# Kernel optimization log

Hardware: AMD Instinct MI355X
Metric: run time of the kernel (lower is better)

## Reference

```python
import jax, jax.numpy as jnp
import numpy as np

N, T = 4, 2048
FEAT, VEC = 512, 16          # feat_size, vec_size
K = 8192                     # codebook_size = prediction_encoder.output_size
CIN = 512                    # prediction_encoder.input_size
OFFSET = 0
IGNORE = -100                # torch CrossEntropyLoss default ignore_index
EPS = 1e-12                  # torch F.normalize eps


def setup_inputs() -> dict:
    key = jax.random.key(0)
    k1, k2, k3, k4, k5, k6 = jax.random.split(key, 6)
    feats = jax.random.normal(k1, (N, T, FEAT), dtype=jnp.float32)
    context = jax.random.normal(k2, (N, T, CIN), dtype=jnp.float32)
    lens = jax.random.randint(k3, (N,), T // 2, T + 1, dtype=jnp.int32)
    # xavier_normal_ for (feat_size, vec_size)
    proj_matrix = jax.random.normal(k4, (FEAT, VEC), dtype=jnp.float32) * np.sqrt(2.0 / (FEAT + VEC))
    cb = jax.random.normal(k5, (K, VEC), dtype=jnp.float32)
    codebook = cb / jnp.maximum(jnp.linalg.norm(cb, axis=1, keepdims=True), EPS)
    W_enc = jax.random.normal(k6, (CIN, K), dtype=jnp.float32) / np.sqrt(CIN)
    b_enc = jnp.zeros((K,), dtype=jnp.float32)
    return {"feats": feats, "context": context, "lens": lens,
            "proj_matrix": proj_matrix, "codebook": codebook,
            "W_enc": W_enc, "b_enc": b_enc}


def reference(feats, context, lens, proj_matrix, codebook, W_enc, b_enc):
    # prediction encoder: Linear(CIN -> K), lens unchanged
    logits = jnp.einsum("ntc,ck->ntk", context, W_enc) + b_enc      # (N,T,K)

    # --- target computation (no_grad in torch) ---
    f = feats[:, OFFSET:] @ proj_matrix                              # (N,T',V)
    f = f / jnp.maximum(jnp.linalg.norm(f, axis=-1, keepdims=True), EPS)
    # squared distance ||f - c||^2 = |f|^2 - 2 f.c + |c|^2; argmin equals
    # argmin of vector_norm since sqrt is monotone. Avoids (N,T,K,V) tensor.
    d2 = (jnp.sum(f * f, axis=-1, keepdims=True)
          - 2.0 * jnp.einsum("ntv,kv->ntk", f, codebook)
          + jnp.sum(codebook * codebook, axis=-1))                   # (N,T',K)
    targets = jnp.argmin(d2, axis=2).astype(jnp.int32)               # (N,T')
    Tp = T - OFFSET
    mask = (lens[:, None] - OFFSET) > jnp.arange(Tp)[None, :]        # (N,T')
    targets = jnp.where(mask, targets, IGNORE)

    # --- masked cross entropy (mean over non-ignored) ---
    logits_f = logits[:, OFFSET:].reshape(-1, K)                     # (N*T',K)
    targets_f = targets.reshape(-1)
    logp = jax.nn.log_softmax(logits_f, axis=-1)
    valid = targets_f != IGNORE
    safe_t = jnp.where(valid, targets_f, 0)
    nll = -jnp.take_along_axis(logp, safe_t[:, None], axis=1)[:, 0]
    loss = jnp.sum(nll * valid) / jnp.maximum(jnp.sum(valid), 1)
    return loss
```

## Files before the change

### kernel.cpp

```cpp
#include <hip/hip_runtime.h>
#include <hip/hip_bf16.h>
#include <hip/hip_fp8.h>

#define MROWS 8192
#define KDIM  512
#define NCOL  8192
#define TSEQ  2048

typedef float f32x4 __attribute__((ext_vector_type(4)));

__device__ __forceinline__ unsigned int pack4_fp8(float a, float b, float c, float d) {
#if __has_builtin(__builtin_amdgcn_cvt_pk_fp8_f32)
  int r = __builtin_amdgcn_cvt_pk_fp8_f32(a, b, 0, false);
  r = __builtin_amdgcn_cvt_pk_fp8_f32(c, d, r, true);
  return (unsigned int)r;
#else
  __hip_fp8_e4m3 ha(a), hb(b), hc(c), hd(d);
  return (unsigned int)ha.__x | ((unsigned int)hb.__x << 8) |
         ((unsigned int)hc.__x << 16) | ((unsigned int)hd.__x << 24);
#endif
}

__device__ __forceinline__ float fp8d(unsigned char b) {
  unsigned int s = b >> 7, e = (b >> 3) & 15, m = b & 7;
  if (e == 0) {
    float v = (float)m * 0.001953125f;
    return s ? -v : v;
  }
  unsigned int bits = (s << 31) | ((e + 120) << 23) | (m << 20);
  return __uint_as_float(bits);
}

__global__ void prep_kernel(const float* __restrict__ X, unsigned char* __restrict__ A8,
                            const float* __restrict__ W, unsigned char* __restrict__ B8,
                            const float* __restrict__ feats, const float* __restrict__ proj,
                            float* __restrict__ F, unsigned long long* __restrict__ amin,
                            float* __restrict__ rowsum) {
  __shared__ float tile[64][65];
  const int tid = threadIdx.x;
  int b = blockIdx.x;
  if (b < 4096) {
    int i = b * 256 + tid;
    float4 v = reinterpret_cast<const float4*>(X)[i];
    reinterpret_cast<unsigned int*>(A8)[i] = pack4_fp8(v.x, v.y, v.z, v.w);
  } else if (b < 5120) {
    b -= 4096;
    const int bx = b & 127, by = b >> 7;
    const int c4 = tid & 15, rr = tid >> 4;
    #pragma unroll
    for (int p = 0; p < 4; ++p) {
      int row = p * 16 + rr;
      float4 v = reinterpret_cast<const float4*>(W + (size_t)(by * 64 + row) * NCOL + bx * 64)[c4];
      tile[row][c4 * 4 + 0] = v.x; tile[row][c4 * 4 + 1] = v.y;
      tile[row][c4 * 4 + 2] = v.z; tile[row][c4 * 4 + 3] = v.w;
    }
    __syncthreads();
    #pragma unroll
    for (int p = 0; p < 4; ++p) {
      int oc = p * 16 + rr;
      unsigned int pk = pack4_fp8(tile[c4 * 4 + 0][oc], tile[c4 * 4 + 1][oc],
                                  tile[c4 * 4 + 2][oc], tile[c4 * 4 + 3][oc]);
      *reinterpret_cast<unsigned int*>(B8 + (size_t)(bx * 64 + oc) * KDIM + by * 64 + c4 * 4) = pk;
    }
  } else if (b < 5632) {
    b -= 5120;
    int rl = tid >> 4, d = tid & 15;
    int row = b * 16 + rl;
    const float4* fr4 = reinterpret_cast<const float4*>(feats + (size_t)row * KDIM);
    float acc = 0.f;
    #pragma unroll 4
    for (int kc = 0; kc < KDIM / 4; ++kc) {
      float4 v = fr4[kc];
      const float* p = proj + (size_t)kc * 64 + d;
      acc += v.x * p[0] + v.y * p[16] + v.z * p[32] + v.w * p[48];
    }
    F[(size_t)row * 16 + d] = acc;
  } else {
    int r = (b - 5632) * 256 + tid;
    amin[r] = ~0ull;
    rowsum[r] = 0.f;
  }
}

#define TGT_BLOCKS 512
#define CB_CODES 128

__device__ __forceinline__ void gld16(const void* g, void* l3) {
  __builtin_amdgcn_global_load_lds((const __attribute__((address_space(1))) void*)g,
                                   (__attribute__((address_space(3))) void*)l3, 16, 0, 0);
}

__global__ __launch_bounds__(256, 4)
void gemm_targets_kernel(const unsigned char* __restrict__ A,
                         const unsigned char* __restrict__ B,
                         const float* __restrict__ bias,
                         float* __restrict__ rowsum,
                         const float* __restrict__ F,
                         const float* __restrict__ cb,
                         unsigned long long* __restrict__ amin) {
  __shared__ __align__(16) unsigned char smem[32768];
  const int tid = threadIdx.x;
  const int bid = blockIdx.x;

  if (bid < TGT_BLOCKS) {
    float (*csh)[16] = (float (*)[16])smem;
    const int r0 = (bid & 7) * 1024 + tid;
    const int c0 = (bid >> 3) * CB_CODES;
    {
      int ci = tid >> 1, half = tid & 1;
      const float4* src = reinterpret_cast<const float4*>(cb + (size_t)(c0 + ci) * 16 + half * 8);
      float4 v0 = src[0], v1 = src[1];
      float4* dst = reinterpret_cast<float4*>(&csh[ci][half * 8]);
      dst[0] = v0; dst[1] = v1;
    }
    float4 fa[4][4];
    #pragma unroll
    for (int q = 0; q < 4; ++q) {
      const float4* fp = reinterpret_cast<const float4*>(F + (size_t)(r0 + q * 256) * 16);
      fa[q][0] = fp[0]; fa[q][1] = fp[1]; fa[q][2] = fp[2]; fa[q][3] = fp[3];
    }
    __syncthreads();

    float best[4] = {3.4e38f, 3.4e38f, 3.4e38f, 3.4e38f};
    int bidx[4] = {0, 0, 0, 0};
    #pragma unroll 2
    for (int ci = 0; ci < CB_CODES; ++ci) {
      const float4* cvp = reinterpret_cast<const float4*>(&csh[ci][0]);
      float4 c0v = cvp[0], c1v = cvp[1], c2v = cvp[2], c3v = cvp[3];
      #pragma unroll
      for (int q = 0; q < 4; ++q) {
        float dot = fa[q][0].x*c0v.x + fa[q][0].y*c0v.y + fa[q][0].z*c0v.z + fa[q][0].w*c0v.w
                  + fa[q][1].x*c1v.x + fa[q][1].y*c1v.y + fa[q][1].z*c1v.z + fa[q][1].w*c1v.w
                  + fa[q][2].x*c2v.x + fa[q][2].y*c2v.y + fa[q][2].z*c2v.z + fa[q][2].w*c2v.w
                  + fa[q][3].x*c3v.x + fa[q][3].y*c3v.y + fa[q][3].z*c3v.z + fa[q][3].w*c3v.w;
        float d = -dot;
        if (d < best[q]) { best[q] = d; bidx[q] = c0 + ci; }
      }
    }
    #pragma unroll
    for (int q = 0; q < 4; ++q) {
      unsigned int u = __float_as_uint(best[q]);
      unsigned int key = (u & 0x80000000u) ? ~u : (u | 0x80000000u);
      unsigned long long pk = ((unsigned long long)key << 32) | (unsigned int)bidx[q];
      atomicMin(&amin[r0 + q * 256], pk);
    }
    return;
  }

  const int gid = bid - TGT_BLOCKS;
  const int wave = tid >> 6;
  const int lane = tid & 63;
  const int xcd = gid & 7, idx = gid >> 3;
  const int bx = xcd * 8 + (idx & 7);
  const int by = idx >> 3;
  const int row0 = by * 128;
  const int col0 = bx * 128;
  const int wr = wave >> 1, wc = wave & 1;
  unsigned char* As = smem;
  unsigned char* Bs = smem + 16384;

  f32x4 acc[4][4];
  #pragma unroll
  for (int i = 0; i < 4; ++i)
    #pragma unroll
    for (int j = 0; j < 4; ++j) acc[i][j] = (f32x4){0.f, 0.f, 0.f, 0.f};

  const int lr = lane >> 2;
  const int lcs = (((lane & 3) ^ ((lane >> 3) & 3)) << 4);

  const int l15 = lane & 15, l16 = lane >> 4;
  const int sw = (l15 >> 1) & 3;
  const int subo = (l16 & 1) * 8;
  const int lg16 = l16 >> 1;

  #pragma unroll
  for (int c = 0; c < 2; ++c) {
    int rchunk = (wave * 2 + c) * 16;
    gld16(A + (size_t)(row0 + rchunk + lr) * KDIM + lcs, As + rchunk * 64);
    gld16(B + (size_t)(col0 + rchunk + lr) * KDIM + lcs, Bs + rchunk * 64);
  }
  __syncthreads();

  #pragma unroll
  for (int t = 0; t < 8; ++t) {
    const int cur = (t & 1) * 8192;
    if (t < 7) {
      const int kt = (t + 1) * 64;
      const int nxt = ((t + 1) & 1) * 8192;
      #pragma unroll
      for (int c = 0; c < 2; ++c) {
        int rchunk = (wave * 2 + c) * 16;
        gld16(A + (size_t)(row0 + rchunk + lr) * KDIM + kt + lcs, As + nxt + rchunk * 64);
        gld16(B + (size_t)(col0 + rchunk + lr) * KDIM + kt + lcs, Bs + nxt + rchunk * 64);
      }
    }
    #pragma unroll
    for (int ks = 0; ks < 2; ++ks) {
      const int poff = (((ks * 2 + lg16) ^ sw) << 4) + subo;
      long af[4], bb[4];
      #pragma unroll
      for (int mi = 0; mi < 4; ++mi)
        af[mi] = *(const long*)(As + cur + (wr * 64 + mi * 16 + l15) * 64 + poff);
      #pragma unroll
      for (int ni = 0; ni < 4; ++ni)
        bb[ni] = *(const long*)(Bs + cur + (wc * 64 + ni * 16 + l15) * 64 + poff);
      #pragma unroll
      for (int mi = 0; mi < 4; ++mi)
        #pragma unroll
        for (int ni = 0; ni < 4; ++ni)
          acc[mi][ni] = __builtin_amdgcn_mfma_f32_16x16x32_fp8_fp8(af[mi], bb[ni], acc[mi][ni], 0, 0, 0);
    }
    if (t < 7) __syncthreads();
  }

  float bv[4];
  #pragma unroll
  for (int ni = 0; ni < 4; ++ni)
    bv[ni] = bias[col0 + wc * 64 + ni * 16 + l15];
  #pragma unroll
  for (int mi = 0; mi < 4; ++mi) {
    int rbase = row0 + wr * 64 + mi * 16 + l16 * 4;
    #pragma unroll
    for (int j = 0; j < 4; ++j) {
      float se = 0.f;
      #pragma unroll
      for (int ni = 0; ni < 4; ++ni)
        se += __expf(acc[mi][ni][j] + bv[ni]);
      #pragma unroll
      for (int o = 1; o < 16; o <<= 1) se += __shfl_xor(se, o);
      if (l15 == 0) atomicAdd(&rowsum[rbase + j], se);
    }
  }
}

__global__ void tgt_logit_kernel(const unsigned char* __restrict__ A,
                                 const unsigned char* __restrict__ B,
                                 const float* __restrict__ bias,
                                 const unsigned long long* __restrict__ amin,
                                 float* __restrict__ tgtlog) {
  const int wv = threadIdx.x >> 6, lane = threadIdx.x & 63;
  const int r = blockIdx.x * 4 + wv;
  const int tg = (int)(amin[r] & 0xffffffffull);
  uint2 ua = reinterpret_cast<const uint2*>(A + (size_t)r * KDIM)[lane];
  uint2 ub = reinterpret_cast<const uint2*>(B + (size_t)tg * KDIM)[lane];
  float s = 0.f;
  const unsigned char* pa = reinterpret_cast<const unsigned char*>(&ua);
  const unsigned char* pb = reinterpret_cast<const unsigned char*>(&ub);
  #pragma unroll
  for (int i = 0; i < 8; ++i) s += fp8d(pa[i]) * fp8d(pb[i]);
  #pragma unroll
  for (int o = 1; o < 64; o <<= 1) s += __shfl_xor(s, o);
  if (lane == 0) tgtlog[r] = s + bias[tg];
}

__global__ void loss_kernel(const float* __restrict__ rowsum, const float* __restrict__ tgtl,
                            const int* __restrict__ lens, float* __restrict__ out) {
  __shared__ float sh[256];
  __shared__ int shc[256];
  int tid = threadIdx.x;
  float s = 0.f; int c = 0;
  for (int r = tid; r < MROWS; r += 256) {
    int n = r >> 11;
    int t = r & (TSEQ - 1);
    if (t < lens[n]) { s += logf(rowsum[r]) - tgtl[r]; c++; }
  }
  sh[tid] = s; shc[tid] = c;
  __syncthreads();
  for (int o = 128; o > 0; o >>= 1) {
    if (tid < o) { sh[tid] += sh[tid + o]; shc[tid] += shc[tid + o]; }
    __syncthreads();
  }
  if (tid == 0) out[0] = sh[0] / (float)max(shc[0], 1);
}

extern "C" void kernel_launch(void* const* d_in, const int* in_sizes, int n_in,
                              void* d_out, int out_size, void* d_ws, size_t ws_size,
                              hipStream_t stream) {
  const float* feats    = (const float*)d_in[0];
  const float* context  = (const float*)d_in[1];
  const int*   lens     = (const int*)d_in[2];
  const float* proj     = (const float*)d_in[3];
  const float* codebook = (const float*)d_in[4];
  const float* W_enc    = (const float*)d_in[5];
  const float* b_enc    = (const float*)d_in[6];
  float* out = (float*)d_out;

  char* ws = (char*)d_ws;
  unsigned char* A8 = (unsigned char*)(ws);
  unsigned char* B8 = (unsigned char*)(ws + 4194304);
  float* F          = (float*)(ws + 8388608);
  unsigned long long* amin = (unsigned long long*)(ws + 8912896);
  float* rowsum     = (float*)(ws + 8978432);
  float* tgtlog     = (float*)(ws + 9011200);

  prep_kernel<<<5664, 256, 0, stream>>>(context, A8, W_enc, B8, feats, proj, F, amin, rowsum);
  gemm_targets_kernel<<<TGT_BLOCKS + 4096, 256, 0, stream>>>(A8, B8, b_enc, rowsum, F, codebook, amin);
  tgt_logit_kernel<<<MROWS / 4, 256, 0, stream>>>(A8, B8, b_enc, amin, tgtlog);
  loss_kernel<<<1, 256, 0, stream>>>(rowsum, tgtlog, lens, out);
}
```

Before: 183.4 us.

## Triple-buffer GEMM K-loop and fuse target-logit with loss reduction

The fp8 GEMM main loop moves to a three-stage LDS ring with prefetch distance two, using explicit vmcnt waits and raw barriers in place of full syncthreads. The separate target-logit kernel and single-block loss kernel are merged into one 64-block kernel that reduces partial losses with an atomicAdd into the output. The output is zeroed in the prep kernel. LDS per GEMM block grows to 48KB, which may reduce occupancy.

```diff
diff --git a/kernel.cpp b/kernel.cpp
--- a/kernel.cpp
+++ b/kernel.cpp
@@ -35,7 +35,7 @@
                             const float* __restrict__ W, unsigned char* __restrict__ B8,
                             const float* __restrict__ feats, const float* __restrict__ proj,
                             float* __restrict__ F, unsigned long long* __restrict__ amin,
-                            float* __restrict__ rowsum) {
+                            float* __restrict__ rowsum, float* __restrict__ out) {
   __shared__ float tile[64][65];
   const int tid = threadIdx.x;
   int b = blockIdx.x;
@@ -79,6 +79,7 @@
     int r = (b - 5632) * 256 + tid;
     amin[r] = ~0ull;
     rowsum[r] = 0.f;
+    if (b == 5632 && tid == 0) out[0] = 0.f;
   }
 }
 
@@ -98,7 +99,7 @@
                          const float* __restrict__ F,
                          const float* __restrict__ cb,
                          unsigned long long* __restrict__ amin) {
-  __shared__ __align__(16) unsigned char smem[32768];
+  __shared__ __align__(16) unsigned char smem[49152];
   const int tid = threadIdx.x;
   const int bid = blockIdx.x;
 
@@ -157,7 +158,7 @@
   const int col0 = bx * 128;
   const int wr = wave >> 1, wc = wave & 1;
   unsigned char* As = smem;
-  unsigned char* Bs = smem + 16384;
+  unsigned char* Bs = smem + 24576;
 
   f32x4 acc[4][4];
   #pragma unroll
@@ -174,19 +175,24 @@
   const int lg16 = l16 >> 1;
 
   #pragma unroll
-  for (int c = 0; c < 2; ++c) {
-    int rchunk = (wave * 2 + c) * 16;
-    gld16(A + (size_t)(row0 + rchunk + lr) * KDIM + lcs, As + rchunk * 64);
-    gld16(B + (size_t)(col0 + rchunk + lr) * KDIM + lcs, Bs + rchunk * 64);
-  }
-  __syncthreads();
+  for (int t0 = 0; t0 < 2; ++t0) {
+    const int kt = t0 * 64, buf = t0 * 8192;
+    #pragma unroll
+    for (int c = 0; c < 2; ++c) {
+      int rchunk = (wave * 2 + c) * 16;
+      gld16(A + (size_t)(row0 + rchunk + lr) * KDIM + kt + lcs, As + buf + rchunk * 64);
+      gld16(B + (size_t)(col0 + rchunk + lr) * KDIM + kt + lcs, Bs + buf + rchunk * 64);
+    }
+  }
+  asm volatile("s_waitcnt vmcnt(4)" ::: "memory");
+  __builtin_amdgcn_s_barrier();
 
   #pragma unroll
   for (int t = 0; t < 8; ++t) {
-    const int cur = (t & 1) * 8192;
-    if (t < 7) {
-      const int kt = (t + 1) * 64;
-      const int nxt = ((t + 1) & 1) * 8192;
+    const int cur = (t % 3) * 8192;
+    if (t + 2 < 8) {
+      const int kt = (t + 2) * 64;
+      const int nxt = ((t + 2) % 3) * 8192;
       #pragma unroll
       for (int c = 0; c < 2; ++c) {
         int rchunk = (wave * 2 + c) * 16;
@@ -210,7 +216,13 @@
         for (int ni = 0; ni < 4; ++ni)
           acc[mi][ni] = __builtin_amdgcn_mfma_f32_16x16x32_fp8_fp8(af[mi], bb[ni], acc[mi][ni], 0, 0, 0);
     }
-    if (t < 7) __syncthreads();
+    if (t < 6) {
+      asm volatile("s_waitcnt vmcnt(4)" ::: "memory");
+      __builtin_amdgcn_s_barrier();
+    } else if (t == 6) {
+      asm volatile("s_waitcnt vmcnt(0)" ::: "memory");
+      __builtin_amdgcn_s_barrier();
+    }
   }
 
   float bv[4];
@@ -233,44 +245,39 @@
   }
 }
 
-__global__ void tgt_logit_kernel(const unsigned char* __restrict__ A,
-                                 const unsigned char* __restrict__ B,
-                                 const float* __restrict__ bias,
-                                 const unsigned long long* __restrict__ amin,
-                                 float* __restrict__ tgtlog) {
-  const int wv = threadIdx.x >> 6, lane = threadIdx.x & 63;
-  const int r = blockIdx.x * 4 + wv;
-  const int tg = (int)(amin[r] & 0xffffffffull);
-  uint2 ua = reinterpret_cast<const uint2*>(A + (size_t)r * KDIM)[lane];
-  uint2 ub = reinterpret_cast<const uint2*>(B + (size_t)tg * KDIM)[lane];
-  float s = 0.f;
-  const unsigned char* pa = reinterpret_cast<const unsigned char*>(&ua);
-  const unsigned char* pb = reinterpret_cast<const unsigned char*>(&ub);
-  #pragma unroll
-  for (int i = 0; i < 8; ++i) s += fp8d(pa[i]) * fp8d(pb[i]);
-  #pragma unroll
-  for (int o = 1; o < 64; o <<= 1) s += __shfl_xor(s, o);
-  if (lane == 0) tgtlog[r] = s + bias[tg];
-}
-
-__global__ void loss_kernel(const float* __restrict__ rowsum, const float* __restrict__ tgtl,
-                            const int* __restrict__ lens, float* __restrict__ out) {
-  __shared__ float sh[256];
-  __shared__ int shc[256];
-  int tid = threadIdx.x;
-  float s = 0.f; int c = 0;
-  for (int r = tid; r < MROWS; r += 256) {
-    int n = r >> 11;
-    int t = r & (TSEQ - 1);
-    if (t < lens[n]) { s += logf(rowsum[r]) - tgtl[r]; c++; }
-  }
-  sh[tid] = s; shc[tid] = c;
+__global__ void tgtloss_kernel(const unsigned char* __restrict__ A,
+                               const unsigned char* __restrict__ B,
+                               const float* __restrict__ bias,
+                               const unsigned long long* __restrict__ amin,
+                               const float* __restrict__ rowsum,
+                               const int* __restrict__ lens,
+                               float* __restrict__ out) {
+  __shared__ float sp[4];
+  const int wave = threadIdx.x >> 6, lane = threadIdx.x & 63;
+  const int cnt = lens[0] + lens[1] + lens[2] + lens[3];
+  const float inv = 1.0f / (float)max(cnt, 1);
+  float partial = 0.f;
+  #pragma unroll 4
+  for (int i = 0; i < 32; ++i) {
+    const int r = blockIdx.x * 128 + wave * 32 + i;
+    const int tg = (int)(amin[r] & 0xffffffffull);
+    uint2 ua = reinterpret_cast<const uint2*>(A + (size_t)r * KDIM)[lane];
+    uint2 ub = reinterpret_cast<const uint2*>(B + (size_t)tg * KDIM)[lane];
+    float s = 0.f;
+    const unsigned char* pa = reinterpret_cast<const unsigned char*>(&ua);
+    const unsigned char* pb = reinterpret_cast<const unsigned char*>(&ub);
+    #pragma unroll
+    for (int k = 0; k < 8; ++k) s += fp8d(pa[k]) * fp8d(pb[k]);
+    #pragma unroll
+    for (int o = 1; o < 64; o <<= 1) s += __shfl_xor(s, o);
+    const int n = r >> 11, t = r & (TSEQ - 1);
+    if (lane == 0 && t < lens[n])
+      partial += logf(rowsum[r]) - (s + bias[tg]);
+  }
+  if (lane == 0) sp[wave] = partial;
   __syncthreads();
-  for (int o = 128; o > 0; o >>= 1) {
-    if (tid < o) { sh[tid] += sh[tid + o]; shc[tid] += shc[tid + o]; }
-    __syncthreads();
-  }
-  if (tid == 0) out[0] = sh[0] / (float)max(shc[0], 1);
+  if (threadIdx.x == 0)
+    atomicAdd(out, (sp[0] + sp[1] + sp[2] + sp[3]) * inv);
 }
 
 extern "C" void kernel_launch(void* const* d_in, const int* in_sizes, int n_in,
@@ -291,10 +298,8 @@
   float* F          = (float*)(ws + 8388608);
   unsigned long long* amin = (unsigned long long*)(ws + 8912896);
   float* rowsum     = (float*)(ws + 8978432);
-  float* tgtlog     = (float*)(ws + 9011200);
-
-  prep_kernel<<<5664, 256, 0, stream>>>(context, A8, W_enc, B8, feats, proj, F, amin, rowsum);
+
+  prep_kernel<<<5664, 256, 0, stream>>>(context, A8, W_enc, B8, feats, proj, F, amin, rowsum, out);
   gemm_targets_kernel<<<TGT_BLOCKS + 4096, 256, 0, stream>>>(A8, B8, b_enc, rowsum, F, codebook, amin);
-  tgt_logit_kernel<<<MROWS / 4, 256, 0, stream>>>(A8, B8, b_enc, amin, tgtlog);
-  loss_kernel<<<1, 256, 0, stream>>>(rowsum, tgtlog, lens, out);
-}
+  tgtloss_kernel<<<64, 256, 0, stream>>>(A8, B8, b_enc, amin, rowsum, lens, out);
+}
```

After: 243.2 us. +32.6%, slower.
